# Performance work log

Hardware: AMD Instinct MI355X
Metric: run time of the kernel (lower is better)

The kernel has to match this reference:

```python
import jax, jax.numpy as jnp
import numpy as np
from jax import lax

NPOINT = 1024
K = 32
EPS = 1e-5  # BatchNorm eps (eval mode, running stats)


def _fps(xyz, npoint):
    """Farthest point sampling. xyz: [B,N,3] -> idx [B,npoint] (int32).
    Deterministic start at index 0 (torch version starts at a random index)."""
    B, N, _ = xyz.shape
    barange = jnp.arange(B)

    def step(carry, _):
        distance, farthest = carry
        centroid = xyz[barange, farthest]                    # [B,3]
        d = jnp.sum((xyz - centroid[:, None, :]) ** 2, -1)   # [B,N]
        distance = jnp.minimum(distance, d)
        new_far = jnp.argmax(distance, axis=-1).astype(jnp.int32)
        return (distance, new_far), farthest

    init = (jnp.full((B, N), 1e10, dtype=xyz.dtype), jnp.zeros((B,), jnp.int32))
    _, centroids = lax.scan(step, init, None, length=npoint)  # [npoint,B]
    return centroids.T                                        # [B,npoint]


def _square_distance(src, dst):
    # src [B,M,3], dst [B,N,3] -> [B,M,N]
    return (jnp.sum(src ** 2, -1)[:, :, None]
            - 2.0 * jnp.einsum('bmc,bnc->bmn', src, dst)
            + jnp.sum(dst ** 2, -1)[:, None, :])


def _gather(p, idx):
    # p [B,N,C], idx [B,...] -> [B,...,C]
    return jax.vmap(lambda pb, ib: pb[ib])(p, idx)


def _mlp_layer(x, w, cb, g, b, m, v):
    # x [B,S,K,Cin]; Conv2d 1x1 == channel matmul, then eval-mode BN, ReLU
    x = jnp.einsum('bskc,oc->bsko', x, w) + cb
    x = (x - m) * (g / jnp.sqrt(v + EPS)) + b
    return jax.nn.relu(x)


def _forward(xyz, points, w0, cb0, g0, b0, m0, v0,
             w1, cb1, g1, b1, m1, v1, w2, cb2, g2, b2, m2, v2):
    fps_idx = _fps(xyz, NPOINT)                       # [B,S]
    new_xyz = _gather(xyz, fps_idx)                   # [B,S,3]
    dists = _square_distance(new_xyz, xyz)            # [B,S,N]
    _, nn_idx = lax.top_k(-dists, K)                  # [B,S,K]
    grouped_xyz = _gather(xyz, nn_idx)                # [B,S,K,3]
    grouped_xyz_norm = grouped_xyz - new_xyz[:, :, None, :]
    grouped_pts = _gather(points, nn_idx)             # [B,S,K,C]
    x = jnp.concatenate([grouped_xyz_norm, grouped_pts], axis=-1)  # [B,S,K,3+C]
    x = _mlp_layer(x, w0, cb0, g0, b0, m0, v0)
    x = _mlp_layer(x, w1, cb1, g1, b1, m1, v1)
    x = _mlp_layer(x, w2, cb2, g2, b2, m2, v2)
    new_points = jnp.max(x, axis=2)                   # max over K -> [B,S,Cout]
    return new_xyz, jnp.transpose(new_points, (0, 2, 1))  # [B,Cout,S]


def setup_inputs() -> dict:
    key = jax.random.key(0)
    ks = jax.random.split(key, 8)
    B, N, C = 16, 4096, 64
    inp = {
        'xyz': jax.random.normal(ks[0], (B, N, 3), jnp.float32),
        'points': jax.random.normal(ks[1], (B, N, C), jnp.float32),
    }
    channels = [(3 + C, 64), (64, 64), (64, 128)]
    for li, (ci, co) in enumerate(channels):
        inp[f'w{li}'] = jax.random.normal(ks[2 + li], (co, ci), jnp.float32) * 0.05
        inp[f'cb{li}'] = jnp.zeros((co,), jnp.float32)
        inp[f'g{li}'] = jnp.ones((co,), jnp.float32)
        inp[f'b{li}'] = jnp.zeros((co,), jnp.float32)
        inp[f'm{li}'] = jnp.zeros((co,), jnp.float32)
        inp[f'v{li}'] = jnp.ones((co,), jnp.float32)
    return inp


def reference(xyz, points, w0, cb0, g0, b0, m0, v0,
              w1, cb1, g1, b1, m1, v1, w2, cb2, g2, b2, m2, v2):
    return _forward(xyz, points, w0, cb0, g0, b0, m0, v0,
                    w1, cb1, g1, b1, m1, v1, w2, cb2, g2, b2, m2, v2)
```

## Files before the change

kernel.cpp:

```cpp
#include <hip/hip_runtime.h>
#include <math.h>

#pragma clang fp contract(off)

#define NPTS 4096
#define NB 16
#define NS 1024
#define KNB 32
#define CPTS 64

#define FLAG_OFF_B  0
#define CNT_OFF_B   64
#define PUBC_OFF_B  128
#define WFRAG_ELEMS 18432
#define NUNITS      16384
#define CAP         256
#define GRAB        2

typedef __attribute__((ext_vector_type(8))) short short8;
typedef __attribute__((ext_vector_type(4))) float f32x4;
typedef __attribute__((ext_vector_type(2))) float f32x2;

__device__ __forceinline__ short f2bf(float f) {
  unsigned u = __float_as_uint(f);
  unsigned r = (u + 0x7fffu + ((u >> 16) & 1u)) >> 16;
  return (short)r;
}

template <int CTRL>
__device__ __forceinline__ int dppmov(int cur) {
  return __builtin_amdgcn_update_dpp(cur, cur, CTRL, 0xF, 0xF, false);
}
template <int CTRL>
__device__ __forceinline__ double dpp_fmax64(double x) {
  int hi = __double2hiint(x), lo = __double2loint(x);
  double o = __hiloint2double(dppmov<CTRL>(hi), dppmov<CTRL>(lo));
  return fmax(x, o);
}
__device__ __forceinline__ double mkkey(float d, unsigned lo) {
  return __hiloint2double((int)__float_as_uint(d), (int)lo);
}

#define XSTR 104
__global__ __launch_bounds__(512, 2) void fused_kernel(
    const float* __restrict__ xyz, const float* __restrict__ points,
    const float* __restrict__ w0, const float* __restrict__ cb0, const float* __restrict__ g0,
    const float* __restrict__ b0, const float* __restrict__ m0, const float* __restrict__ v0,
    const float* __restrict__ w1, const float* __restrict__ cb1, const float* __restrict__ g1,
    const float* __restrict__ b1, const float* __restrict__ m1, const float* __restrict__ v1,
    const float* __restrict__ w2, const float* __restrict__ cb2, const float* __restrict__ g2,
    const float* __restrict__ b2, const float* __restrict__ m2, const float* __restrict__ v2,
    char* __restrict__ wsb, float* __restrict__ newxyz, float* __restrict__ outp) {
  struct FpsSh {
    float4 sxyz4[NPTS];
    float4 centL[NS];
    unsigned long long part[2][8];
  };
  struct WorkerSh {
    short Wlds[WFRAG_ELEMS];
    short X[8][32 * XSTR];
    unsigned long long cand[8][CAP];
    int nnL[8][KNB];
    float biasL[256];
    unsigned cnt[8];
  };
  __shared__ union { FpsSh f; WorkerSh w; } sh;

  const int t = threadIdx.x;
  const int lane = t & 63;
  const int wave = t >> 6;
  unsigned* flagp = (unsigned*)(wsb + FLAG_OFF_B);
  unsigned* cntp  = (unsigned*)(wsb + CNT_OFF_B);
  float* pubC = (float*)(wsb + PUBC_OFF_B);

  if (blockIdx.x < NB) {
    const int b = blockIdx.x;
    const float* xb = xyz + (size_t)b * NPTS * 3;
    float* outb = newxyz + (size_t)b * NS * 3;

    for (int i = t; i < NPTS; i += 512)
      sh.f.sxyz4[i] = make_float4(xb[i * 3 + 0], xb[i * 3 + 1], xb[i * 3 + 2], 0.f);

    f32x2 px2[4], py2[4], pz2[4], d2[4];
    unsigned lo8[8];
#pragma unroll
    for (int j = 0; j < 8; ++j) lo8[j] = ~(unsigned)(t + 512 * j);
#pragma unroll
    for (int j2 = 0; j2 < 4; ++j2) {
      int n0 = t + 512 * (2 * j2), n1 = t + 512 * (2 * j2 + 1);
      px2[j2].x = xb[n0 * 3 + 0]; px2[j2].y = xb[n1 * 3 + 0];
      py2[j2].x = xb[n0 * 3 + 1]; py2[j2].y = xb[n1 * 3 + 1];
      pz2[j2].x = xb[n0 * 3 + 2]; pz2[j2].y = xb[n1 * 3 + 2];
      d2[j2].x = 1e10f; d2[j2].y = 1e10f;
    }
    __syncthreads();
    float cx = sh.f.sxyz4[0].x, cy = sh.f.sxyz4[0].y, cz = sh.f.sxyz4[0].z;
    if (t == 0) sh.f.centL[0] = sh.f.sxyz4[0];

    for (int it = 1; it < NS; ++it) {
      const int buf = it & 1;
      f32x2 cax; cax.x = cx; cax.y = cx;
      f32x2 cay; cay.x = cy; cay.y = cy;
      f32x2 caz; caz.x = cz; caz.y = cz;
      double kk[8];
#pragma unroll
      for (int j2 = 0; j2 < 4; ++j2) {
        f32x2 dx = px2[j2] - cax;
        f32x2 dy = py2[j2] - cay;
        f32x2 dz = pz2[j2] - caz;
        f32x2 dd = (dx * dx + dy * dy) + dz * dz;
        f32x2 dv = d2[j2];
        dv.x = fminf(dv.x, dd.x);
        dv.y = fminf(dv.y, dd.y);
        d2[j2] = dv;
        kk[2 * j2]     = mkkey(dv.x, lo8[2 * j2]);
        kk[2 * j2 + 1] = mkkey(dv.y, lo8[2 * j2 + 1]);
      }
      double km = fmax(fmax(fmax(kk[0], kk[1]), fmax(kk[2], kk[3])),
                       fmax(fmax(kk[4], kk[5]), fmax(kk[6], kk[7])));
      km = dpp_fmax64<0xB1>(km);  km = dpp_fmax64<0x4E>(km);  km = dpp_fmax64<0x141>(km);
      km = dpp_fmax64<0x140>(km); km = dpp_fmax64<0x142>(km); km = dpp_fmax64<0x143>(km);
      if (lane == 63)
        sh.f.part[buf][wave] = (unsigned long long)__double_as_longlong(km);
      __syncthreads();
      double kw = __longlong_as_double((long long)sh.f.part[buf][lane & 7]);
      kw = dpp_fmax64<0xB1>(kw); kw = dpp_fmax64<0x4E>(kw); kw = dpp_fmax64<0x141>(kw);
      int bi = (int)(~(unsigned)__double2loint(kw)) & 4095;
      float4 c4 = sh.f.sxyz4[bi];
      cx = c4.x; cy = c4.y; cz = c4.z;
      if (t == 0) sh.f.centL[it] = c4;
      if ((it & 31) == 31 && wave == 0) {
        if (lane == 0) {
          asm volatile("s_waitcnt vmcnt(0)" ::: "memory");
          __hip_atomic_store(&flagp[b], (unsigned)(it - 31), __ATOMIC_RELAXED, __HIP_MEMORY_SCOPE_AGENT);
        }
        if (lane < 32) {
          int ci = it - 31 + lane;
          float4 cc = sh.f.centL[ci];
          float* dst = pubC + ((size_t)b * NS + ci) * 3;
          __hip_atomic_store(dst + 0, cc.x, __ATOMIC_RELAXED, __HIP_MEMORY_SCOPE_AGENT);
          __hip_atomic_store(dst + 1, cc.y, __ATOMIC_RELAXED, __HIP_MEMORY_SCOPE_AGENT);
          __hip_atomic_store(dst + 2, cc.z, __ATOMIC_RELAXED, __HIP_MEMORY_SCOPE_AGENT);
        }
      }
    }
    if (wave == 0 && lane == 0) {
      asm volatile("s_waitcnt vmcnt(0)" ::: "memory");
      __hip_atomic_store(&flagp[b], (unsigned)NS, __ATOMIC_RELAXED, __HIP_MEMORY_SCOPE_AGENT);
    }
    __syncthreads();
    const float* cf = (const float*)sh.f.centL;
    for (int i = t; i < NS * 3; i += 512) {
      int p = i / 3, c = i - p * 3;
      outb[i] = cf[p * 4 + c];
    }
  }

  __syncthreads();
  for (int i = t; i < WFRAG_ELEMS; i += 512) {
    int g = i >> 9, ln = (i >> 3) & 63, j = i & 7;
    int l, nt, s;
    if (g < 12)      { l = 0; nt = g / 3;  s = g % 3; }
    else if (g < 20) { l = 1; int gg = g - 12; nt = gg >> 1; s = gg & 1; }
    else             { l = 2; int gg = g - 20; nt = gg >> 1; s = gg & 1; }
    int n = nt * 16 + (ln & 15);
    int k = s * 32 + ((ln >> 4) << 3) + j;
    float val = 0.f;
    if (l == 0) {
      float sc = g0[n] / sqrtf(v0[n] + 1e-5f);
      if (k < 64)      val = w0[n * 67 + (k + 3)] * sc;
      else if (k < 67) val = w0[n * 67 + (k - 64)] * sc;
    }
    else if (l == 1) { val = w1[n * 64 + k] * (g1[n] / sqrtf(v1[n] + 1e-5f)); }
    else { val = w2[n * 64 + k] * (g2[n] / sqrtf(v2[n] + 1e-5f)); }
    sh.w.Wlds[i] = f2bf(val);
  }
  if (t < 256) {
    int o = t;
    float bv;
    if (o < 64)       { float sc = g0[o] / sqrtf(v0[o] + 1e-5f); bv = (cb0[o] - m0[o]) * sc + b0[o]; }
    else if (o < 128) { int c = o - 64;  float sc = g1[c] / sqrtf(v1[c] + 1e-5f); bv = (cb1[c] - m1[c]) * sc + b1[c]; }
    else              { int c = o - 128; float sc = g2[c] / sqrtf(v2[c] + 1e-5f); bv = (cb2[c] - m2[c]) * sc + b2[c]; }
    sh.w.biasL[o] = bv;
  }
  __syncthreads();

  unsigned long long* cand = sh.w.cand[wave];
  for (int i = lane; i < (32 * XSTR) / 2; i += 64) ((int*)sh.w.X[wave])[i] = 0;

  unsigned fcache = 0;

  for (;;) {
    unsigned base = 0;
    if (lane == 0) base = atomicAdd(cntp, (unsigned)GRAB);
    base = (unsigned)__builtin_amdgcn_readfirstlane((int)base);
    if (base >= NUNITS) break;
    unsigned uend = base + GRAB;
    if (uend > NUNITS) uend = NUNITS;

    for (unsigned u = base; u < uend; ++u) {
    const int b = (int)(u & 15u);
    const int s = (int)(u >> 4);

    {
      unsigned need = (unsigned)s + 1u;
      unsigned have = (unsigned)__shfl((int)fcache, b, 64);
      if (have < need) {
        unsigned f;
        for (;;) {
          f = __hip_atomic_load(&flagp[b], __ATOMIC_RELAXED, __HIP_MEMORY_SCOPE_AGENT);
          if (f >= need) break;
          __builtin_amdgcn_s_sleep(64);
        }
        if (lane == b) fcache = f;
        asm volatile("" ::: "memory");
      }
    }
    const float* qcp = pubC + ((size_t)b * NS + s) * 3;
    float qx = __hip_atomic_load(qcp + 0, __ATOMIC_RELAXED, __HIP_MEMORY_SCOPE_AGENT);
    float qy = __hip_atomic_load(qcp + 1, __ATOMIC_RELAXED, __HIP_MEMORY_SCOPE_AGENT);
    float qz = __hip_atomic_load(qcp + 2, __ATOMIC_RELAXED, __HIP_MEMORY_SCOPE_AGENT);

    const float* xb = xyz + (size_t)b * NPTS * 3;
    float s2 = __fadd_rn(__fadd_rn(__fmul_rn(qx, qx), __fmul_rn(qy, qy)), __fmul_rn(qz, qz));

    unsigned long long mkey = 0xFFFFFFFFFFFFFFFFull;
#pragma unroll 4
    for (int j = 0; j < 64; ++j) {
      int n = j * 64 + lane;
      float px = xb[n * 3], py = xb[n * 3 + 1], pz = xb[n * 3 + 2];
      float n2 = __fadd_rn(__fadd_rn(__fmul_rn(px, px), __fmul_rn(py, py)), __fmul_rn(pz, pz));
      float dt = __fadd_rn(__fadd_rn(__fmul_rn(qx, px), __fmul_rn(qy, py)), __fmul_rn(qz, pz));
      float d  = __fadd_rn(__fsub_rn(s2, __fmul_rn(2.0f, dt)), n2);
      unsigned uu = __float_as_uint(d);
      uu ^= (0x80000000u | (unsigned)((int)uu >> 31));
      unsigned long long key = ((unsigned long long)uu << 32) | (unsigned)n;
      mkey = key < mkey ? key : mkey;
    }

    {
      unsigned mh = (unsigned)(mkey >> 32), ml2 = (unsigned)mkey;
#pragma unroll
      for (int k = 2; k <= 64; k <<= 1) {
#pragma unroll
        for (int j = k >> 1; j >= 1; j >>= 1) {
          unsigned oh = (unsigned)__shfl_xor((int)mh, j, 64);
          unsigned ol = (unsigned)__shfl_xor((int)ml2, j, 64);
          bool up = (lane & k) == 0;
          bool lower = (lane & j) == 0;
          bool omin = (oh < mh) || (oh == mh && ol < ml2);
          bool keep_o = (lower == up) ? omin : !omin;
          mh = keep_o ? oh : mh;
          ml2 = keep_o ? ol : ml2;
        }
      }
      unsigned th = (unsigned)__builtin_amdgcn_readlane((int)mh, 31);
      unsigned tl = (unsigned)__builtin_amdgcn_readlane((int)ml2, 31);
      mkey = ((unsigned long long)th << 32) | tl;
    }
    const unsigned long long tau = mkey;

    if (lane == 0) sh.w.cnt[wave] = 0;
    asm volatile("s_waitcnt lgkmcnt(0)" ::: "memory");
#pragma unroll 4
    for (int j = 0; j < 64; ++j) {
      int n = j * 64 + lane;
      float px = xb[n * 3], py = xb[n * 3 + 1], pz = xb[n * 3 + 2];
      float n2 = __fadd_rn(__fadd_rn(__fmul_rn(px, px), __fmul_rn(py, py)), __fmul_rn(pz, pz));
      float dt = __fadd_rn(__fadd_rn(__fmul_rn(qx, px), __fmul_rn(qy, py)), __fmul_rn(qz, pz));
      float d  = __fadd_rn(__fsub_rn(s2, __fmul_rn(2.0f, dt)), n2);
      unsigned uu = __float_as_uint(d);
      uu ^= (0x80000000u | (unsigned)((int)uu >> 31));
      unsigned long long key = ((unsigned long long)uu << 32) | (unsigned)n;
      if (key <= tau) {
        unsigned pos = atomicAdd(&sh.w.cnt[wave], 1u);
        if (pos < CAP) cand[pos] = key;
      }
    }
    asm volatile("s_waitcnt lgkmcnt(0)" ::: "memory");
    unsigned cn = sh.w.cnt[wave];
    if (cn > CAP) cn = CAP;

    for (unsigned bb = 0; bb < cn; bb += 64) {
      unsigned i = bb + (unsigned)lane;
      unsigned long long ki = (i < cn) ? cand[i] : 0xFFFFFFFFFFFFFFFFull;
      int rank = 0;
#pragma unroll 4
      for (unsigned c2 = 0; c2 < cn; ++c2)
        rank += (cand[c2] < ki) ? 1 : 0;
      if (i < cn && rank < KNB) sh.w.nnL[wave][rank] = (int)(unsigned)(ki & 0xFFFFFFFFull);
    }
    asm volatile("s_waitcnt lgkmcnt(0)" ::: "memory");

    {
      const int qi = wave;
      const float* pb = points + (size_t)b * NPTS * CPTS;
      const float* bias = sh.w.biasL;
      short* X = sh.w.X[qi];

      {
        int h = lane & 1, r = lane >> 1;
        int idx = sh.w.nnL[qi][r];
        const f32x4* src = (const f32x4*)(pb + (size_t)idx * CPTS) + h * 8;
        short8* dst = (short8*)&X[r * XSTR + h * 32];
#pragma unroll
        for (int q = 0; q < 4; ++q) {
          f32x4 v0 = src[q * 2], v1 = src[q * 2 + 1];
          short8 o;
          o[0] = f2bf(v0[0]); o[1] = f2bf(v0[1]); o[2] = f2bf(v0[2]); o[3] = f2bf(v0[3]);
          o[4] = f2bf(v1[0]); o[5] = f2bf(v1[1]); o[6] = f2bf(v1[2]); o[7] = f2bf(v1[3]);
          dst[q] = o;
        }
      }
      if (lane < 32) {
        int idx = sh.w.nnL[qi][lane];
        X[lane * XSTR + 64] = f2bf(__fsub_rn(xb[idx * 3 + 0], qx));
        X[lane * XSTR + 65] = f2bf(__fsub_rn(xb[idx * 3 + 1], qy));
        X[lane * XSTR + 66] = f2bf(__fsub_rn(xb[idx * 3 + 2], qz));
      }

      const int ml = lane & 15, quad = lane >> 4;
      const short8* Wf = (const short8*)sh.w.Wlds;

      short8 a0[2][3];
#pragma unroll
      for (int m2 = 0; m2 < 2; ++m2)
#pragma unroll
        for (int s3 = 0; s3 < 3; ++s3)
          a0[m2][s3] = *(const short8*)&X[(m2 * 16 + ml) * XSTR + s3 * 32 + quad * 8];
      f32x4 acc0[2][4];
#pragma unroll
      for (int m2 = 0; m2 < 2; ++m2)
#pragma unroll
        for (int nt = 0; nt < 4; ++nt) {
          f32x4 c = {0.f, 0.f, 0.f, 0.f};
#pragma unroll
          for (int s3 = 0; s3 < 3; ++s3)
            c = __builtin_amdgcn_mfma_f32_16x16x32_bf16(a0[m2][s3], Wf[(nt * 3 + s3) * 64 + lane], c, 0, 0, 0);
          acc0[m2][nt] = c;
        }
#pragma unroll
      for (int m2 = 0; m2 < 2; ++m2)
#pragma unroll
        for (int nt = 0; nt < 4; ++nt) {
          int ch = nt * 16 + ml;
          float bv = bias[ch];
#pragma unroll
          for (int r4 = 0; r4 < 4; ++r4) {
            float y = fmaxf(acc0[m2][nt][r4] + bv, 0.f);
            int m = quad * 4 + r4;
            int sK = ch >> 5, qq = (ch >> 3) & 3, jj = ch & 7;
            X[((m2 * 2 + sK) * 64 + qq * 16 + m) * 8 + jj] = f2bf(y);
          }
        }

      short8 a1[2][2];
#pragma unroll
      for (int m2 = 0; m2 < 2; ++m2)
#pragma unroll
        for (int sK = 0; sK < 2; ++sK)
          a1[m2][sK] = *(const short8*)&X[((m2 * 2 + sK) * 64 + lane) * 8];
      f32x4 acc1[2][4];
#pragma unroll
      for (int m2 = 0; m2 < 2; ++m2)
#pragma unroll
        for (int nt = 0; nt < 4; ++nt) {
          f32x4 c = {0.f, 0.f, 0.f, 0.f};
#pragma unroll
          for (int sK = 0; sK < 2; ++sK)
            c = __builtin_amdgcn_mfma_f32_16x16x32_bf16(a1[m2][sK], Wf[(12 + nt * 2 + sK) * 64 + lane], c, 0, 0, 0);
          acc1[m2][nt] = c;
        }
#pragma unroll
      for (int m2 = 0; m2 < 2; ++m2)
#pragma unroll
        for (int nt = 0; nt < 4; ++nt) {
          int ch = nt * 16 + ml;
          float bv = bias[64 + ch];
#pragma unroll
          for (int r4 = 0; r4 < 4; ++r4) {
            float y = fmaxf(acc1[m2][nt][r4] + bv, 0.f);
            int m = quad * 4 + r4;
            int sK = ch >> 5, qq = (ch >> 3) & 3, jj = ch & 7;
            X[((m2 * 2 + sK) * 64 + qq * 16 + m) * 8 + jj] = f2bf(y);
          }
        }

      short8 a2[2][2];
#pragma unroll
      for (int m2 = 0; m2 < 2; ++m2)
#pragma unroll
        for (int sK = 0; sK < 2; ++sK)
          a2[m2][sK] = *(const short8*)&X[((m2 * 2 + sK) * 64 + lane) * 8];
#pragma unroll
      for (int nt = 0; nt < 8; ++nt) {
        f32x4 c0 = {0.f, 0.f, 0.f, 0.f}, c1 = {0.f, 0.f, 0.f, 0.f};
        short8 w0f = Wf[(20 + nt * 2 + 0) * 64 + lane];
        short8 w1f = Wf[(20 + nt * 2 + 1) * 64 + lane];
        c0 = __builtin_amdgcn_mfma_f32_16x16x32_bf16(a2[0][0], w0f, c0, 0, 0, 0);
        c0 = __builtin_amdgcn_mfma_f32_16x16x32_bf16(a2[0][1], w1f, c0, 0, 0, 0);
        c1 = __builtin_amdgcn_mfma_f32_16x16x32_bf16(a2[1][0], w0f, c1, 0, 0, 0);
        c1 = __builtin_amdgcn_mfma_f32_16x16x32_bf16(a2[1][1], w1f, c1, 0, 0, 0);
        float bv = bias[128 + nt * 16 + ml];
        float m = -1.f;
#pragma unroll
        for (int r4 = 0; r4 < 4; ++r4) {
          m = fmaxf(m, fmaxf(c0[r4] + bv, 0.f));
          m = fmaxf(m, fmaxf(c1[r4] + bv, 0.f));
        }
        m = fmaxf(m, __shfl_xor(m, 16, 64));
        m = fmaxf(m, __shfl_xor(m, 32, 64));
        if (lane < 16) outp[((size_t)b * 128 + nt * 16 + lane) * NS + s] = m;
      }
    }
    }
  }
}

extern "C" void kernel_launch(void* const* d_in, const int* in_sizes, int n_in,
                              void* d_out, int out_size, void* d_ws, size_t ws_size,
                              hipStream_t stream) {
  const float* xyz    = (const float*)d_in[0];
  const float* points = (const float*)d_in[1];
  const float* w0  = (const float*)d_in[2];
  const float* cb0 = (const float*)d_in[3];
  const float* g0  = (const float*)d_in[4];
  const float* b0  = (const float*)d_in[5];
  const float* m0  = (const float*)d_in[6];
  const float* v0  = (const float*)d_in[7];
  const float* w1  = (const float*)d_in[8];
  const float* cb1 = (const float*)d_in[9];
  const float* g1  = (const float*)d_in[10];
  const float* b1  = (const float*)d_in[11];
  const float* m1  = (const float*)d_in[12];
  const float* v1  = (const float*)d_in[13];
  const float* w2  = (const float*)d_in[14];
  const float* cb2 = (const float*)d_in[15];
  const float* g2  = (const float*)d_in[16];
  const float* b2  = (const float*)d_in[17];
  const float* m2  = (const float*)d_in[18];
  const float* v2  = (const float*)d_in[19];

  char*  wsb    = (char*)d_ws;
  float* newxyz = (float*)d_out;
  float* outp   = (float*)d_out + (size_t)NB * NS * 3;

  hipMemsetAsync(wsb, 0, 128, stream);
  fused_kernel<<<256, 512, 0, stream>>>(
      xyz, points, w0, cb0, g0, b0, m0, v0, w1, cb1, g1, b1, m1, v1,
      w2, cb2, g2, b2, m2, v2, wsb, newxyz, outp);
}
```

Measured before the change: 880.3 us.

## Run FPS in a single wave with ballot argmax, shrink blocks to 4 waves

New measurement: 2.139 ms. +143.0%, slower.

```diff
diff --git a/kernel.cpp b/kernel.cpp
--- a/kernel.cpp
+++ b/kernel.cpp
@@ -16,6 +16,8 @@
 #define NUNITS      16384
 #define CAP         256
 #define GRAB        2
+#define NWAVES      4
+#define GRID        248
 
 typedef __attribute__((ext_vector_type(8))) short short8;
 typedef __attribute__((ext_vector_type(4))) float f32x4;
@@ -32,17 +34,12 @@
   return __builtin_amdgcn_update_dpp(cur, cur, CTRL, 0xF, 0xF, false);
 }
 template <int CTRL>
-__device__ __forceinline__ double dpp_fmax64(double x) {
-  int hi = __double2hiint(x), lo = __double2loint(x);
-  double o = __hiloint2double(dppmov<CTRL>(hi), dppmov<CTRL>(lo));
-  return fmax(x, o);
+__device__ __forceinline__ void dpp_fmax(float& m) {
+  m = fmaxf(m, __int_as_float(dppmov<CTRL>(__float_as_int(m))));
 }
-__device__ __forceinline__ double mkkey(float d, unsigned lo) {
-  return __hiloint2double((int)__float_as_uint(d), (int)lo);
-}
 
 #define XSTR 104
-__global__ __launch_bounds__(512, 2) void fused_kernel(
+__global__ __launch_bounds__(256, 1) void fused_kernel(
     const float* __restrict__ xyz, const float* __restrict__ points,
     const float* __restrict__ w0, const float* __restrict__ cb0, const float* __restrict__ g0,
     const float* __restrict__ b0, const float* __restrict__ m0, const float* __restrict__ v0,
@@ -54,15 +51,14 @@
   struct FpsSh {
     float4 sxyz4[NPTS];
     float4 centL[NS];
-    unsigned long long part[2][8];
   };
   struct WorkerSh {
     short Wlds[WFRAG_ELEMS];
-    short X[8][32 * XSTR];
-    unsigned long long cand[8][CAP];
-    int nnL[8][KNB];
+    short X[NWAVES][32 * XSTR];
+    unsigned long long cand[NWAVES][CAP];
+    int nnL[NWAVES][KNB];
     float biasL[256];
-    unsigned cnt[8];
+    unsigned cnt[NWAVES];
   };
   __shared__ union { FpsSh f; WorkerSh w; } sh;
 
@@ -74,37 +70,34 @@
   float* pubC = (float*)(wsb + PUBC_OFF_B);
 
   if (blockIdx.x < NB) {
+    if (wave != 0) return;
     const int b = blockIdx.x;
     const float* xb = xyz + (size_t)b * NPTS * 3;
     float* outb = newxyz + (size_t)b * NS * 3;
 
-    for (int i = t; i < NPTS; i += 512)
+    for (int i = lane; i < NPTS; i += 64)
       sh.f.sxyz4[i] = make_float4(xb[i * 3 + 0], xb[i * 3 + 1], xb[i * 3 + 2], 0.f);
 
-    f32x2 px2[4], py2[4], pz2[4], d2[4];
-    unsigned lo8[8];
-#pragma unroll
-    for (int j = 0; j < 8; ++j) lo8[j] = ~(unsigned)(t + 512 * j);
-#pragma unroll
-    for (int j2 = 0; j2 < 4; ++j2) {
-      int n0 = t + 512 * (2 * j2), n1 = t + 512 * (2 * j2 + 1);
+    f32x2 px2[32], py2[32], pz2[32], d2[32];
+#pragma unroll
+    for (int j2 = 0; j2 < 32; ++j2) {
+      int n0 = (2 * j2) * 64 + lane, n1 = (2 * j2 + 1) * 64 + lane;
       px2[j2].x = xb[n0 * 3 + 0]; px2[j2].y = xb[n1 * 3 + 0];
       py2[j2].x = xb[n0 * 3 + 1]; py2[j2].y = xb[n1 * 3 + 1];
       pz2[j2].x = xb[n0 * 3 + 2]; pz2[j2].y = xb[n1 * 3 + 2];
       d2[j2].x = 1e10f; d2[j2].y = 1e10f;
     }
-    __syncthreads();
-    float cx = sh.f.sxyz4[0].x, cy = sh.f.sxyz4[0].y, cz = sh.f.sxyz4[0].z;
-    if (t == 0) sh.f.centL[0] = sh.f.sxyz4[0];
+    float4 c0 = sh.f.sxyz4[0];
+    float cx = c0.x, cy = c0.y, cz = c0.z;
+    if (lane == 0) sh.f.centL[0] = c0;
 
     for (int it = 1; it < NS; ++it) {
-      const int buf = it & 1;
       f32x2 cax; cax.x = cx; cax.y = cx;
       f32x2 cay; cay.x = cy; cay.y = cy;
       f32x2 caz; caz.x = cz; caz.y = cz;
-      double kk[8];
-#pragma unroll
-      for (int j2 = 0; j2 < 4; ++j2) {
+      f32x2 dm2; dm2.x = -1.f; dm2.y = -1.f;
+#pragma unroll
+      for (int j2 = 0; j2 < 32; ++j2) {
         f32x2 dx = px2[j2] - cax;
         f32x2 dy = py2[j2] - cay;
         f32x2 dz = pz2[j2] - caz;
@@ -113,51 +106,52 @@
         dv.x = fminf(dv.x, dd.x);
         dv.y = fminf(dv.y, dd.y);
         d2[j2] = dv;
-        kk[2 * j2]     = mkkey(dv.x, lo8[2 * j2]);
-        kk[2 * j2 + 1] = mkkey(dv.y, lo8[2 * j2 + 1]);
-      }
-      double km = fmax(fmax(fmax(kk[0], kk[1]), fmax(kk[2], kk[3])),
-                       fmax(fmax(kk[4], kk[5]), fmax(kk[6], kk[7])));
-      km = dpp_fmax64<0xB1>(km);  km = dpp_fmax64<0x4E>(km);  km = dpp_fmax64<0x141>(km);
-      km = dpp_fmax64<0x140>(km); km = dpp_fmax64<0x142>(km); km = dpp_fmax64<0x143>(km);
-      if (lane == 63)
-        sh.f.part[buf][wave] = (unsigned long long)__double_as_longlong(km);
-      __syncthreads();
-      double kw = __longlong_as_double((long long)sh.f.part[buf][lane & 7]);
-      kw = dpp_fmax64<0xB1>(kw); kw = dpp_fmax64<0x4E>(kw); kw = dpp_fmax64<0x141>(kw);
-      int bi = (int)(~(unsigned)__double2loint(kw)) & 4095;
-      float4 c4 = sh.f.sxyz4[bi];
-      cx = c4.x; cy = c4.y; cz = c4.z;
-      if (t == 0) sh.f.centL[it] = c4;
-      if ((it & 31) == 31 && wave == 0) {
+        dm2.x = fmaxf(dm2.x, dv.x);
+        dm2.y = fmaxf(dm2.y, dv.y);
+      }
+      float m = fmaxf(dm2.x, dm2.y);
+      dpp_fmax<0xB1>(m);  dpp_fmax<0x4E>(m);  dpp_fmax<0x141>(m);
+      dpp_fmax<0x140>(m); dpp_fmax<0x142>(m); dpp_fmax<0x143>(m);
+      float M = __int_as_float(__builtin_amdgcn_readlane(__float_as_int(m), 63));
+      int bestn = 0;
+#pragma unroll
+      for (int j2 = 31; j2 >= 0; --j2) {
+        unsigned long long my = __ballot(d2[j2].y == M);
+        bestn = my ? ((2 * j2 + 1) * 64 + (int)__ffsll((long long)my) - 1) : bestn;
+        unsigned long long mx = __ballot(d2[j2].x == M);
+        bestn = mx ? ((2 * j2) * 64 + (int)__ffsll((long long)mx) - 1) : bestn;
+      }
+      float4 cc = sh.f.sxyz4[bestn];
+      cx = cc.x; cy = cc.y; cz = cc.z;
+      if (lane == 0) sh.f.centL[it] = cc;
+      if ((it & 31) == 31) {
         if (lane == 0) {
           asm volatile("s_waitcnt vmcnt(0)" ::: "memory");
           __hip_atomic_store(&flagp[b], (unsigned)(it - 31), __ATOMIC_RELAXED, __HIP_MEMORY_SCOPE_AGENT);
         }
         if (lane < 32) {
           int ci = it - 31 + lane;
-          float4 cc = sh.f.centL[ci];
+          float4 cv = sh.f.centL[ci];
           float* dst = pubC + ((size_t)b * NS + ci) * 3;
-          __hip_atomic_store(dst + 0, cc.x, __ATOMIC_RELAXED, __HIP_MEMORY_SCOPE_AGENT);
-          __hip_atomic_store(dst + 1, cc.y, __ATOMIC_RELAXED, __HIP_MEMORY_SCOPE_AGENT);
-          __hip_atomic_store(dst + 2, cc.z, __ATOMIC_RELAXED, __HIP_MEMORY_SCOPE_AGENT);
-        }
-      }
-    }
-    if (wave == 0 && lane == 0) {
+          __hip_atomic_store(dst + 0, cv.x, __ATOMIC_RELAXED, __HIP_MEMORY_SCOPE_AGENT);
+          __hip_atomic_store(dst + 1, cv.y, __ATOMIC_RELAXED, __HIP_MEMORY_SCOPE_AGENT);
+          __hip_atomic_store(dst + 2, cv.z, __ATOMIC_RELAXED, __HIP_MEMORY_SCOPE_AGENT);
+        }
+      }
+    }
+    if (lane == 0) {
       asm volatile("s_waitcnt vmcnt(0)" ::: "memory");
       __hip_atomic_store(&flagp[b], (unsigned)NS, __ATOMIC_RELAXED, __HIP_MEMORY_SCOPE_AGENT);
     }
-    __syncthreads();
     const float* cf = (const float*)sh.f.centL;
-    for (int i = t; i < NS * 3; i += 512) {
+    for (int i = lane; i < NS * 3; i += 64) {
       int p = i / 3, c = i - p * 3;
       outb[i] = cf[p * 4 + c];
     }
+    return;
   }
 
-  __syncthreads();
-  for (int i = t; i < WFRAG_ELEMS; i += 512) {
+  for (int i = t; i < WFRAG_ELEMS; i += 256) {
     int g = i >> 9, ln = (i >> 3) & 63, j = i & 7;
     int l, nt, s;
     if (g < 12)      { l = 0; nt = g / 3;  s = g % 3; }
@@ -175,7 +169,7 @@
     else { val = w2[n * 64 + k] * (g2[n] / sqrtf(v2[n] + 1e-5f)); }
     sh.w.Wlds[i] = f2bf(val);
   }
-  if (t < 256) {
+  {
     int o = t;
     float bv;
     if (o < 64)       { float sc = g0[o] / sqrtf(v0[o] + 1e-5f); bv = (cb0[o] - m0[o]) * sc + b0[o]; }
@@ -446,7 +440,7 @@
   float* outp   = (float*)d_out + (size_t)NB * NS * 3;
 
   hipMemsetAsync(wsb, 0, 128, stream);
-  fused_kernel<<<256, 512, 0, stream>>>(
+  fused_kernel<<<GRID, 256, 0, stream>>>(
       xyz, points, w0, cb0, g0, b0, m0, v0, w1, cb1, g1, b1, m1, v1,
       w2, cb2, g2, b2, m2, v2, wsb, newxyz, outp);
 }
```
